# Optimization experiments

Hardware: AMD Instinct MI355X
Metric: run time of the kernel (lower is better)

Reference implementation:

```python
import jax, jax.numpy as jnp
import numpy as np

B, L, D, H = 16, 1024, 1024, 16
HD = D // H  # head dim = 64


def setup_inputs() -> dict:
    rng = jax.random.key(0)
    ks = jax.random.split(rng, 12)
    s = 0.02
    return {
        "key": jax.random.normal(ks[0], (B, L, D), jnp.float32),
        "value": jax.random.normal(ks[1], (B, L, D), jnp.float32),
        "query": jax.random.normal(ks[2], (B, L, D), jnp.float32),
        "atten_masks": jax.random.randint(ks[3], (B, L, L), 0, 2, jnp.int32),
        "Wk": jax.random.normal(ks[4], (D, D), jnp.float32) * s,
        "bk": jnp.zeros((D,), jnp.float32),
        "Wq": jax.random.normal(ks[5], (D, D), jnp.float32) * s,
        "bq": jnp.zeros((D,), jnp.float32),
        "Wv": jax.random.normal(ks[6], (D, D), jnp.float32) * s,
        "bv": jnp.zeros((D,), jnp.float32),
        "Wp": jax.random.normal(ks[7], (D, D), jnp.float32) * s,
        "bp": jnp.zeros((D,), jnp.float32),
    }


def reference(key, value, query, atten_masks, Wk, bk, Wq, bq, Wv, bv, Wp, bp):
    # Linear projections (torch nn.Linear: x @ W^T + b)
    def lin(x, W, b):
        return x @ W.T + b

    # [B, L, D] -> [B, H, L, HD]
    def heads(x):
        return x.reshape(B, L, H, HD).transpose(0, 2, 1, 3)

    k = heads(lin(key, Wk, bk))
    q = heads(lin(query, Wq, bq))
    v = heads(lin(value, Wv, bv))

    scale = 1.0 / np.sqrt(HD).astype(np.float32)
    att = jnp.einsum("bhqd,bhkd->bhqk", q, k) * scale  # [B, H, L, L]
    att = jnp.where(atten_masks[:, None, :, :] == 0, -jnp.inf, att)
    att = jax.nn.softmax(att, axis=-1)

    y = jnp.einsum("bhqk,bhkd->bhqd", att, v)  # [B, H, L, HD]
    y = y.transpose(0, 2, 1, 3).reshape(B, L, D)
    return lin(y, Wp, bp)
```

## Files before the change

### kernel.cpp

```cpp
#include <hip/hip_runtime.h>

typedef __bf16 bf16_t;
typedef __bf16 bf16x4 __attribute__((ext_vector_type(4)));
typedef __bf16 bf16x8 __attribute__((ext_vector_type(8)));
typedef float f32x4 __attribute__((ext_vector_type(4)));
typedef float f32x16 __attribute__((ext_vector_type(16)));
typedef unsigned u32x2 __attribute__((ext_vector_type(2)));

#define QSCALE 0.18033688f

__device__ __forceinline__ int swz(int row) { return (row ^ (row >> 3)) & 7; }
__device__ __forceinline__ int swz2(int row) { return (row ^ (row >> 2)) & 3; }
__device__ __forceinline__ int swzv(int row) { return (row ^ (row >> 3)) & 15; }

__device__ __forceinline__ f32x4 mfma16(bf16x8 a, bf16x8 b, f32x4 c) {
  return __builtin_amdgcn_mfma_f32_16x16x32_bf16(a, b, c, 0, 0, 0);
}
__device__ __forceinline__ f32x16 mfma32(bf16x8 a, bf16x8 b, f32x16 c) {
  return __builtin_amdgcn_mfma_f32_32x32x16_bf16(a, b, c, 0, 0, 0);
}

__device__ __forceinline__ void gl_lds16(const void* g, void* l) {
  __builtin_amdgcn_global_load_lds(
      (const __attribute__((address_space(1))) unsigned int*)g,
      (__attribute__((address_space(3))) unsigned int*)l, 16, 0, 0);
}

__global__ __launch_bounds__(256) void cvt_all_kernel(
    const float* __restrict__ key, const float* __restrict__ query,
    const float* __restrict__ value, const float* __restrict__ Wk,
    const float* __restrict__ Wq, const float* __restrict__ Wv,
    const float* __restrict__ Wp, const int* __restrict__ mask,
    bf16_t* __restrict__ I1, bf16_t* __restrict__ I2, bf16_t* __restrict__ I3,
    bf16_t* __restrict__ Wkb, bf16_t* __restrict__ Wqb,
    bf16_t* __restrict__ Wvb, bf16_t* __restrict__ Wpb,
    unsigned* __restrict__ mbits) {
  const int bid = blockIdx.x;
  if (bid >= 53248) {
    int idx = (bid - 53248) * 256 + threadIdx.x;
    const int4* src = (const int4*)(mask + (size_t)idx * 32);
    unsigned w = 0;
#pragma unroll
    for (int i = 0; i < 8; ++i) {
      int4 v = src[i];
      w |= (v.x != 0 ? 1u : 0u) << (i * 4 + 0);
      w |= (v.y != 0 ? 1u : 0u) << (i * 4 + 1);
      w |= (v.z != 0 ? 1u : 0u) << (i * 4 + 2);
      w |= (v.w != 0 ? 1u : 0u) << (i * 4 + 3);
    }
    mbits[idx] = w;
    return;
  }
  const float* s;
  bf16_t* d;
  int base;
  float sc = 1.0f;
  if (bid < 16384) { s = key; d = I1; base = bid; }
  else if (bid < 32768) { s = query; d = I2; base = bid - 16384; }
  else if (bid < 49152) { s = value; d = I3; base = bid - 32768; }
  else if (bid < 50176) { s = Wk; d = Wkb; base = bid - 49152; }
  else if (bid < 51200) { s = Wq; d = Wqb; base = bid - 50176; sc = QSCALE; }
  else if (bid < 52224) { s = Wv; d = Wvb; base = bid - 51200; }
  else { s = Wp; d = Wpb; base = bid - 52224; }
  int i = base * 256 + threadIdx.x;
  float4 v = ((const float4*)s)[i];
  bf16x4 o;
  o[0] = (bf16_t)(v.x * sc); o[1] = (bf16_t)(v.y * sc);
  o[2] = (bf16_t)(v.z * sc); o[3] = (bf16_t)(v.w * sc);
  ((bf16x4*)d)[i] = o;
}

template <typename OT>
__device__ __forceinline__ void gemm256_body(const bf16_t* __restrict__ A,
                                             const bf16_t* __restrict__ W,
                                             const float* __restrict__ bias,
                                             float bscale,
                                             OT* __restrict__ O) {
  extern __shared__ __align__(16) char smem[];
  bf16_t* AsBase = (bf16_t*)smem;
  bf16_t* BsBase = (bf16_t*)(smem + 3 * 8192 * 2);

  const int t = threadIdx.x;
  const int lane = t & 63;
  const int wid = t >> 6;
  const int g = lane >> 4;
  const int lr = lane & 15;
  const int wm = wid >> 2, wn = wid & 3;
  const int lid = blockIdx.x;
  const int logical = (lid & 7) * 32 + (lid >> 3);
  const int m0 = (logical >> 2) * 256;
  const int n0 = (logical & 3) * 256;

  f32x4 acc[8][4] = {};

  auto STAGE = [&](int buf, int kb) {
    bf16_t* Ab = AsBase + buf * 8192;
    bf16_t* Bb = BsBase + buf * 8192;
#pragma unroll
    for (int rr = 0; rr < 2; ++rr) {
      int s = rr * 512 + t;
      int row = s >> 2, c = s & 3;
      gl_lds16(A + (size_t)(m0 + row) * 1024 + kb + (c ^ swz2(row)) * 8,
               &Ab[(rr * 512 + wid * 64) * 8]);
      gl_lds16(W + (size_t)(n0 + row) * 1024 + kb + (c ^ swz2(row)) * 8,
               &Bb[(rr * 512 + wid * 64) * 8]);
    }
  };

  STAGE(0, 0);
  STAGE(1, 32);

  int cur = 0;
  for (int kb = 0; kb < 1024; kb += 32) {
    if (kb + 32 < 1024)
      asm volatile("s_waitcnt vmcnt(4)" ::: "memory");
    else
      asm volatile("s_waitcnt vmcnt(0)" ::: "memory");
    __builtin_amdgcn_sched_barrier(0);
    __builtin_amdgcn_s_barrier();
    __builtin_amdgcn_sched_barrier(0);

    if (kb + 64 < 1024) {
      int fut = cur + 2;
      if (fut >= 3) fut -= 3;
      STAGE(fut, kb + 64);
    }

    const bf16_t* Ab = AsBase + cur * 8192;
    const bf16_t* Bb = BsBase + cur * 8192;
    bf16x8 a[8], b[4];
#pragma unroll
    for (int i = 0; i < 8; ++i) {
      int row = wm * 128 + i * 16 + lr;
      a[i] = *(const bf16x8*)&Ab[row * 32 + ((g ^ swz2(row))) * 8];
    }
#pragma unroll
    for (int j = 0; j < 4; ++j) {
      int row = wn * 64 + j * 16 + lr;
      b[j] = *(const bf16x8*)&Bb[row * 32 + ((g ^ swz2(row))) * 8];
    }
    __builtin_amdgcn_s_setprio(1);
#pragma unroll
    for (int i = 0; i < 8; ++i)
#pragma unroll
      for (int j = 0; j < 4; ++j)
        acc[i][j] = mfma16(a[i], b[j], acc[i][j]);
    __builtin_amdgcn_s_setprio(0);

    cur = cur + 1;
    if (cur >= 3) cur -= 3;
  }

  float bval[4];
#pragma unroll
  for (int j = 0; j < 4; ++j)
    bval[j] = bias[n0 + wn * 64 + j * 16 + lr] * bscale;
#pragma unroll
  for (int i = 0; i < 8; ++i)
#pragma unroll
    for (int r = 0; r < 4; ++r) {
      int row = m0 + wm * 128 + i * 16 + g * 4 + r;
#pragma unroll
      for (int j = 0; j < 4; ++j) {
        int n = n0 + wn * 64 + j * 16 + lr;
        O[(size_t)row * 1024 + n] = (OT)(acc[i][j][r] + bval[j]);
      }
    }
}

__global__ __launch_bounds__(512, 2) void gemm256_qkv_kernel(
    const bf16_t* key, const bf16_t* query, const bf16_t* value,
    const bf16_t* Wkb, const bf16_t* Wqb, const bf16_t* Wvb, const float* bk,
    const float* bq, const float* bv, bf16_t* ko, bf16_t* qo, bf16_t* vo) {
  const bf16_t *A, *W;
  const float* bi;
  bf16_t* O;
  float bs = 1.0f;
  if (blockIdx.y == 0) { A = key; W = Wkb; bi = bk; O = ko; }
  else if (blockIdx.y == 1) { A = query; W = Wqb; bi = bq; O = qo; bs = QSCALE; }
  else { A = value; W = Wvb; bi = bv; O = vo; }
  gemm256_body<bf16_t>(A, W, bi, bs, O);
}

__global__ __launch_bounds__(512, 2) void gemm256_out_kernel(
    const bf16_t* __restrict__ A, const bf16_t* __restrict__ W,
    const float* __restrict__ b, float* __restrict__ O) {
  gemm256_body<float>(A, W, b, 1.0f, O);
}

__global__ __launch_bounds__(256) void transpose_v_kernel(
    const bf16_t* __restrict__ v_ws, bf16_t* __restrict__ vT) {
  __shared__ bf16_t T[64 * 66];
  const int kc = blockIdx.x, h = blockIdx.y, b = blockIdx.z;
  const int t = threadIdx.x;
  {
    int key = t >> 2, dblk = t & 3;
    const bf16_t* src =
        v_ws + ((size_t)(b * 1024 + kc * 64 + key)) * 1024 + h * 64 + dblk * 16;
    bf16x8 a0 = *(const bf16x8*)src;
    bf16x8 a1 = *(const bf16x8*)(src + 8);
    bf16_t* row = &T[key * 66 + dblk * 16];
#pragma unroll
    for (int j = 0; j < 4; ++j) {
      ((unsigned*)row)[j] = ((const unsigned*)&a0)[j];
      ((unsigned*)row)[j + 4] = ((const unsigned*)&a1)[j];
    }
  }
  __syncthreads();
  {
    int d = t >> 2, kcl = t & 3;
    bf16x8 o0, o1;
#pragma unroll
    for (int e = 0; e < 8; ++e) {
      o0[e] = T[(kcl * 16 + e) * 66 + d];
      o1[e] = T[(kcl * 16 + 8 + e) * 66 + d];
    }
    bf16_t* dst =
        vT + ((size_t)((b * 16 + h) * 64 + d)) * 1024 + kc * 64 + kcl * 16;
    *(bf16x8*)dst = o0;
    *(bf16x8*)(dst + 8) = o1;
  }
}

__global__ __launch_bounds__(512) void attn_kernel(
    const bf16_t* __restrict__ q_ws, const bf16_t* __restrict__ k_ws,
    const bf16_t* __restrict__ vT, const unsigned* __restrict__ mbits,
    bf16_t* __restrict__ y_ws) {
  __shared__ __align__(16) bf16_t Ks[128 * 64];
  __shared__ __align__(16) bf16_t Vs[64 * 128];

  const int lid = blockIdx.x;
  const int logical = (lid & 7) * 128 + (lid >> 3);
  const int qb = logical & 3;
  const int h = (logical >> 2) & 15;
  const int b = logical >> 6;
  const int t = threadIdx.x, lane = t & 63, wid = t >> 6;
  const int ql = lane & 31;
  const int hh = lane >> 5;
  const int q = qb * 256 + wid * 32 + ql;

  bf16x8 qf[4];
  {
    const bf16_t* qp = q_ws + ((size_t)(b * 1024 + q)) * 1024 + h * 64 + hh * 8;
#pragma unroll
    for (int kc = 0; kc < 4; ++kc) qf[kc] = *(const bf16x8*)(qp + kc * 16);
  }

  bf16x8 onesf;
#pragma unroll
  for (int e = 0; e < 8; ++e) onesf[e] = (bf16_t)1.0f;

  f32x16 acc0 = {}, acc1 = {}, accl = {};
  const bf16_t* Kb = k_ws + ((size_t)b * 1024) * 1024 + h * 64;
  const bf16_t* Vb = vT + ((size_t)((b * 16 + h) * 64)) * 1024;
  const unsigned* mrow = mbits + ((size_t)(b * 1024 + q)) * 32;

  for (int kb = 0; kb < 8; ++kb) {
    __syncthreads();
#pragma unroll
    for (int rr = 0; rr < 2; ++rr) {
      int s = rr * 512 + t;
      int row = s >> 3, c = s & 7;
      gl_lds16(Kb + (size_t)(kb * 128 + row) * 1024 + (c ^ swz(row)) * 8,
               &Ks[(rr * 512 + wid * 64) * 8]);
    }
#pragma unroll
    for (int rr = 0; rr < 2; ++rr) {
      int s = rr * 512 + t;
      int row = s >> 4, c = s & 15;
      gl_lds16(Vb + (size_t)row * 1024 + kb * 128 + ((c ^ swzv(row))) * 8,
               &Vs[(rr * 512 + wid * 64) * 8]);
    }
    uint4 mw = *(const uint4*)&mrow[kb * 4];
    __syncthreads();

#pragma unroll
    for (int ct = 0; ct < 4; ++ct) {
      f32x16 c = {};
      __builtin_amdgcn_s_setprio(1);
#pragma unroll
      for (int kc = 0; kc < 4; ++kc) {
        int row = ct * 32 + ql;
        bf16x8 kf = *(const bf16x8*)&Ks[row * 64 + (((kc * 2 + hh) ^ swz(row))) * 8];
        c = mfma32(kf, qf[kc], c);
      }
      __builtin_amdgcn_s_setprio(0);

      unsigned w = ((const unsigned*)&mw)[ct] >> (4 * hh);
      float p[16];
#pragma unroll
      for (int r = 0; r < 16; ++r) {
        const int posr = (r & 3) + 8 * (r >> 2);
        int nm = (int)(w << (31 - posr)) >> 31;
        float e0 = __builtin_amdgcn_exp2f(c[r]);
        p[r] = __int_as_float(__float_as_int(e0) & nm);
      }

      bf16x8 pbt[2];
#pragma unroll
      for (int j = 0; j < 2; ++j) {
        const int base = j * 8;
        union { bf16_t h[2]; unsigned u; } a0, a1, b0, b1;
        a0.h[0] = (bf16_t)p[base + 0]; a0.h[1] = (bf16_t)p[base + 1];
        a1.h[0] = (bf16_t)p[base + 2]; a1.h[1] = (bf16_t)p[base + 3];
        b0.h[0] = (bf16_t)p[base + 4]; b0.h[1] = (bf16_t)p[base + 5];
        b1.h[0] = (bf16_t)p[base + 6]; b1.h[1] = (bf16_t)p[base + 7];
        u32x2 s0 = __builtin_amdgcn_permlane32_swap(a0.u, b0.u, false, false);
        u32x2 s1 = __builtin_amdgcn_permlane32_swap(a1.u, b1.u, false, false);
        union { unsigned u[4]; bf16x8 v; } pk;
        pk.u[0] = s0.x;
        pk.u[1] = s1.x;
        pk.u[2] = s0.y;
        pk.u[3] = s1.y;
        pbt[j] = pk.v;
      }

      __builtin_amdgcn_s_setprio(1);
#pragma unroll
      for (int j = 0; j < 2; ++j) {
        int sl = (2 * ct + j) * 2 + hh;
        {
          int row = ql;
          bf16x8 vf = *(const bf16x8*)&Vs[row * 128 + ((sl ^ swzv(row))) * 8];
          acc0 = mfma32(vf, pbt[j], acc0);
        }
        {
          int row = 32 + ql;
          bf16x8 vf = *(const bf16x8*)&Vs[row * 128 + ((sl ^ swzv(row))) * 8];
          acc1 = mfma32(vf, pbt[j], acc1);
        }
        accl = mfma32(onesf, pbt[j], accl);
      }
      __builtin_amdgcn_s_setprio(0);
    }
  }

  float inv = 1.0f / fmaxf(accl[0], 1e-30f);
  bf16_t* yp = y_ws + ((size_t)(b * 1024 + q)) * 1024 + h * 64;
#pragma unroll
  for (int j = 0; j < 4; ++j) {
    bf16x4 o0, o1;
#pragma unroll
    for (int e = 0; e < 4; ++e) {
      o0[e] = (bf16_t)(acc0[4 * j + e] * inv);
      o1[e] = (bf16_t)(acc1[4 * j + e] * inv);
    }
    *(bf16x4*)&yp[8 * j + 4 * hh] = o0;
    *(bf16x4*)&yp[32 + 8 * j + 4 * hh] = o1;
  }
}

extern "C" void kernel_launch(void* const* d_in, const int* in_sizes, int n_in,
                              void* d_out, int out_size, void* d_ws,
                              size_t ws_size, hipStream_t stream) {
  (void)in_sizes; (void)n_in; (void)out_size; (void)ws_size;
  const float* key = (const float*)d_in[0];
  const float* value = (const float*)d_in[1];
  const float* query = (const float*)d_in[2];
  const int* mask = (const int*)d_in[3];
  const float* Wk = (const float*)d_in[4];
  const float* bk = (const float*)d_in[5];
  const float* Wq = (const float*)d_in[6];
  const float* bq = (const float*)d_in[7];
  const float* Wv = (const float*)d_in[8];
  const float* bv = (const float*)d_in[9];
  const float* Wp = (const float*)d_in[10];
  const float* bp = (const float*)d_in[11];
  float* out = (float*)d_out;

  char* ws = (char*)d_ws;
  const size_t MB = 1ull << 20;
  unsigned* mbits = (unsigned*)(ws);
  bf16_t* Wkb = (bf16_t*)(ws + 2 * MB);
  bf16_t* Wqb = (bf16_t*)(ws + 4 * MB);
  bf16_t* Wvb = (bf16_t*)(ws + 6 * MB);
  bf16_t* Wpb = (bf16_t*)(ws + 8 * MB);
  bf16_t* I1 = (bf16_t*)(ws + 10 * MB);
  bf16_t* I2 = (bf16_t*)(ws + 42 * MB);
  bf16_t* I3 = (bf16_t*)(ws + 74 * MB);
  bf16_t* k_ws = (bf16_t*)(ws + 106 * MB);
  bf16_t* q_ws = (bf16_t*)(ws + 138 * MB);
  bf16_t* v_ws = (bf16_t*)(ws + 170 * MB);
  bf16_t* vT_ws = I1;
  bf16_t* y_ws = I2;

  const size_t GEMM_LDS = 3 * 8192 * 2 * 2;

  cvt_all_kernel<<<55296, 256, 0, stream>>>(key, query, value, Wk, Wq, Wv, Wp,
                                            mask, I1, I2, I3, Wkb, Wqb, Wvb,
                                            Wpb, mbits);
  gemm256_qkv_kernel<<<dim3(256, 3), 512, GEMM_LDS, stream>>>(
      I1, I2, I3, Wkb, Wqb, Wvb, bk, bq, bv, k_ws, q_ws, v_ws);
  transpose_v_kernel<<<dim3(16, 16, 16), 256, 0, stream>>>(v_ws, vT_ws);
  attn_kernel<<<1024, 512, 0, stream>>>(q_ws, k_ws, vT_ws, mbits, y_ws);
  gemm256_out_kernel<<<256, 512, GEMM_LDS, stream>>>(y_ws, Wpb, bp, out);
}
```

Before: 344.3 us.

## Restructure GEMM mainloop to double-buffered K=64 tiles with quarter-step staging

```diff
diff --git a/kernel.cpp b/kernel.cpp
--- a/kernel.cpp
+++ b/kernel.cpp
@@ -10,7 +10,6 @@
 #define QSCALE 0.18033688f
 
 __device__ __forceinline__ int swz(int row) { return (row ^ (row >> 3)) & 7; }
-__device__ __forceinline__ int swz2(int row) { return (row ^ (row >> 2)) & 3; }
 __device__ __forceinline__ int swzv(int row) { return (row ^ (row >> 3)) & 15; }
 
 __device__ __forceinline__ f32x4 mfma16(bf16x8 a, bf16x8 b, f32x4 c) {
@@ -78,7 +77,7 @@
                                              OT* __restrict__ O) {
   extern __shared__ __align__(16) char smem[];
   bf16_t* AsBase = (bf16_t*)smem;
-  bf16_t* BsBase = (bf16_t*)(smem + 3 * 8192 * 2);
+  bf16_t* BsBase = (bf16_t*)(smem + 2 * 16384 * 2);
 
   const int t = threadIdx.x;
   const int lane = t & 63;
@@ -93,62 +92,94 @@
 
   f32x4 acc[8][4] = {};
 
-  auto STAGE = [&](int buf, int kb) {
-    bf16_t* Ab = AsBase + buf * 8192;
-    bf16_t* Bb = BsBase + buf * 8192;
+  auto STAGE_A = [&](int buf, int kb, int h) {
+    bf16_t* Ab = AsBase + buf * 16384;
 #pragma unroll
     for (int rr = 0; rr < 2; ++rr) {
       int s = rr * 512 + t;
-      int row = s >> 2, c = s & 3;
-      gl_lds16(A + (size_t)(m0 + row) * 1024 + kb + (c ^ swz2(row)) * 8,
-               &Ab[(rr * 512 + wid * 64) * 8]);
-      gl_lds16(W + (size_t)(n0 + row) * 1024 + kb + (c ^ swz2(row)) * 8,
-               &Bb[(rr * 512 + wid * 64) * 8]);
+      int l = s >> 3, c = s & 7;
+      int row = ((l >> 6) << 7) + h * 64 + (l & 63);
+      int lb = rr * 64 + wid * 8;
+      int rowb = ((lb >> 6) << 7) + h * 64 + (lb & 63);
+      gl_lds16(A + (size_t)(m0 + row) * 1024 + kb + (c ^ swz(row)) * 8,
+               &Ab[rowb * 64]);
     }
   };
-
-  STAGE(0, 0);
-  STAGE(1, 32);
-
-  int cur = 0;
-  for (int kb = 0; kb < 1024; kb += 32) {
-    if (kb + 32 < 1024)
-      asm volatile("s_waitcnt vmcnt(4)" ::: "memory");
-    else
-      asm volatile("s_waitcnt vmcnt(0)" ::: "memory");
-    __builtin_amdgcn_sched_barrier(0);
-    __builtin_amdgcn_s_barrier();
-    __builtin_amdgcn_sched_barrier(0);
-
-    if (kb + 64 < 1024) {
-      int fut = cur + 2;
-      if (fut >= 3) fut -= 3;
-      STAGE(fut, kb + 64);
-    }
-
-    const bf16_t* Ab = AsBase + cur * 8192;
-    const bf16_t* Bb = BsBase + cur * 8192;
-    bf16x8 a[8], b[4];
-#pragma unroll
-    for (int i = 0; i < 8; ++i) {
-      int row = wm * 128 + i * 16 + lr;
-      a[i] = *(const bf16x8*)&Ab[row * 32 + ((g ^ swz2(row))) * 8];
-    }
-#pragma unroll
-    for (int j = 0; j < 4; ++j) {
-      int row = wn * 64 + j * 16 + lr;
-      b[j] = *(const bf16x8*)&Bb[row * 32 + ((g ^ swz2(row))) * 8];
-    }
-    __builtin_amdgcn_s_setprio(1);
-#pragma unroll
-    for (int i = 0; i < 8; ++i)
-#pragma unroll
-      for (int j = 0; j < 4; ++j)
-        acc[i][j] = mfma16(a[i], b[j], acc[i][j]);
-    __builtin_amdgcn_s_setprio(0);
-
-    cur = cur + 1;
-    if (cur >= 3) cur -= 3;
+  auto STAGE_B = [&](int buf, int kb, int h) {
+    bf16_t* Bb = BsBase + buf * 16384;
+#pragma unroll
+    for (int rr = 0; rr < 2; ++rr) {
+      int s = rr * 512 + t;
+      int l = s >> 3, c = s & 7;
+      int row = ((l >> 5) << 6) + h * 32 + (l & 31);
+      int lb = rr * 64 + wid * 8;
+      int rowb = ((lb >> 5) << 6) + h * 32 + (lb & 31);
+      gl_lds16(W + (size_t)(n0 + row) * 1024 + kb + (c ^ swz(row)) * 8,
+               &Bb[rowb * 64]);
+    }
+  };
+  auto STAGE_HALF = [&](int buf, int kb, int which) {
+    if (which == 0) STAGE_A(buf, kb, 0);
+    else if (which == 1) STAGE_B(buf, kb, 0);
+    else if (which == 2) STAGE_B(buf, kb, 1);
+    else STAGE_A(buf, kb, 1);
+  };
+
+  STAGE_HALF(0, 0, 0);
+  STAGE_HALF(0, 0, 1);
+  STAGE_HALF(0, 0, 2);
+  STAGE_HALF(0, 0, 3);
+
+  for (int kb = 0; kb < 1024; kb += 64) {
+    const int cur = (kb >> 6) & 1;
+    const bool more = kb + 64 < 1024;
+    const bf16_t* Ab = AsBase + cur * 16384;
+    const bf16_t* Bb = BsBase + cur * 16384;
+
+#pragma unroll
+    for (int p = 0; p < 4; ++p) {
+      const int ih = p >> 1, jh = p & 1;
+      if (more) {
+        asm volatile("s_waitcnt vmcnt(4)" ::: "memory");
+      } else {
+        if (p == 0)      asm volatile("s_waitcnt vmcnt(4)" ::: "memory");
+        else if (p == 1) asm volatile("s_waitcnt vmcnt(2)" ::: "memory");
+        else             asm volatile("s_waitcnt vmcnt(0)" ::: "memory");
+      }
+      __builtin_amdgcn_sched_barrier(0);
+      __builtin_amdgcn_s_barrier();
+      __builtin_amdgcn_sched_barrier(0);
+
+      if (more) STAGE_HALF(cur ^ 1, kb + 64, p);
+
+      bf16x8 a[4][2], b[2][2];
+#pragma unroll
+      for (int i = 0; i < 4; ++i) {
+        int row = wm * 128 + (ih * 4 + i) * 16 + lr;
+#pragma unroll
+        for (int kk = 0; kk < 2; ++kk)
+          a[i][kk] =
+              *(const bf16x8*)&Ab[row * 64 + (((kk * 4 + g) ^ swz(row))) * 8];
+      }
+#pragma unroll
+      for (int j = 0; j < 2; ++j) {
+        int row = wn * 64 + (jh * 2 + j) * 16 + lr;
+#pragma unroll
+        for (int kk = 0; kk < 2; ++kk)
+          b[j][kk] =
+              *(const bf16x8*)&Bb[row * 64 + (((kk * 4 + g) ^ swz(row))) * 8];
+      }
+      __builtin_amdgcn_s_setprio(1);
+#pragma unroll
+      for (int i = 0; i < 4; ++i)
+#pragma unroll
+        for (int j = 0; j < 2; ++j)
+#pragma unroll
+          for (int kk = 0; kk < 2; ++kk)
+            acc[ih * 4 + i][jh * 2 + j] =
+                mfma16(a[i][kk], b[j][kk], acc[ih * 4 + i][jh * 2 + j]);
+      __builtin_amdgcn_s_setprio(0);
+    }
   }
 
   float bval[4];
@@ -384,7 +415,7 @@
   bf16_t* vT_ws = I1;
   bf16_t* y_ws = I2;
 
-  const size_t GEMM_LDS = 3 * 8192 * 2 * 2;
+  const size_t GEMM_LDS = 2 * 16384 * 2 * 2;
 
   cvt_all_kernel<<<55296, 256, 0, stream>>>(key, query, value, Wk, Wq, Wv, Wp,
                                             mask, I1, I2, I3, Wkb, Wqb, Wvb,
```

After: 368.9 us. 1.07x slower.
